# Performance work log

Measured on AMD Instinct MI355X. Metric: run time of the kernel, lower is better.

Reference implementation:

```python
import jax, jax.numpy as jnp
import numpy as np

B, S, D = 1, 4096, 1024
H, DH = 8, 128
SCALING = 256.0 ** -0.5
SOFTCAP = 50.0
WINDOW = 512
EPS = 1e-6
NEG = -1e30


def setup_inputs() -> dict:
    key = jax.random.key(0)
    ks = jax.random.split(key, 8)
    hidden_states = jax.random.normal(ks[0], (B, S, D), dtype=jnp.float32)
    # rope tables: plausible cos/sin in [-1,1]
    inv_freq = 1.0 / (10000.0 ** (jnp.arange(0, DH, 2, dtype=jnp.float32) / DH))
    t = jnp.arange(S, dtype=jnp.float32)
    freqs = jnp.outer(t, inv_freq)  # [S, DH/2]
    emb = jnp.concatenate([freqs, freqs], axis=-1)  # [S, DH]
    cos = jnp.cos(emb)[None]  # [1, S, DH]
    sin = jnp.sin(emb)[None]
    w = 0.02
    Wq = jax.random.normal(ks[1], (H * DH, D), dtype=jnp.float32) * w
    Wk = jax.random.normal(ks[2], (H * DH, D), dtype=jnp.float32) * w
    Wv = jax.random.normal(ks[3], (H * DH, D), dtype=jnp.float32) * w
    Wo = jax.random.normal(ks[4], (D, H * DH), dtype=jnp.float32) * w
    q_norm_w = jnp.zeros((DH,), dtype=jnp.float32)
    k_norm_w = jnp.zeros((DH,), dtype=jnp.float32)
    return {"hidden_states": hidden_states, "cos": cos, "sin": sin,
            "Wq": Wq, "Wk": Wk, "Wv": Wv, "Wo": Wo,
            "q_norm_w": q_norm_w, "k_norm_w": k_norm_w}


def _rms_norm(x, w):
    # Gemma3 RMSNorm: x * rsqrt(mean(x^2) + eps) * (1 + w)
    var = jnp.mean(jnp.square(x), axis=-1, keepdims=True)
    return x * jax.lax.rsqrt(var + EPS) * (1.0 + w)


def _rotate_half(x):
    x1, x2 = jnp.split(x, 2, axis=-1)
    return jnp.concatenate([-x2, x1], axis=-1)


def reference(hidden_states, cos, sin, Wq, Wk, Wv, Wo, q_norm_w, k_norm_w):
    b, s, _ = hidden_states.shape
    # QKV projections -> [B, H, S, DH]
    q = (hidden_states @ Wq.T).reshape(b, s, H, DH).transpose(0, 2, 1, 3)
    k = (hidden_states @ Wk.T).reshape(b, s, H, DH).transpose(0, 2, 1, 3)
    v = (hidden_states @ Wv.T).reshape(b, s, H, DH).transpose(0, 2, 1, 3)
    # per-head RMSNorm on q and k
    q = _rms_norm(q, q_norm_w)
    k = _rms_norm(k, k_norm_w)
    # RoPE (cos/sin broadcast over heads via unsqueeze(1))
    c = cos[:, None, :, :]
    si = sin[:, None, :, :]
    q = q * c + _rotate_half(q) * si
    k = k * c + _rotate_half(k) * si
    # scores with scaling and logit softcapping
    scores = jnp.einsum('bhqd,bhkd->bhqk', q, k) * SCALING
    scores = SOFTCAP * jnp.tanh(scores / SOFTCAP)
    # causal + sliding-window mask: attend to j with 0 <= i - j < WINDOW (plus j == i)
    i = jnp.arange(s)[:, None]
    j = jnp.arange(s)[None, :]
    mask = (j <= i) & (i - j < WINDOW)  # [S, S]
    scores = jnp.where(mask[None, None], scores, NEG)
    probs = jax.nn.softmax(scores, axis=-1)  # [B, H, S, S]
    attn = jnp.einsum('bhqk,bhkd->bhqd', probs, v)
    attn = attn.transpose(0, 2, 1, 3).reshape(b, s, H * DH)
    out = attn @ Wo.T
    return out, probs
```

## Files before the change

### kernel.cpp

```cpp
#include <hip/hip_runtime.h>

#define S_LEN 4096

typedef _Float16 f16;
typedef __bf16 bf16;
typedef __attribute__((ext_vector_type(4))) _Float16 f16x4;
typedef __attribute__((ext_vector_type(8))) _Float16 f16x8;
typedef __attribute__((ext_vector_type(8))) __bf16 bf16x8;
typedef __attribute__((ext_vector_type(4))) float f32x4;

__device__ __forceinline__ void async_cp16(void* lds, const void* g) {
  __builtin_amdgcn_global_load_lds((const __attribute__((address_space(1))) void*)g,
                                   (__attribute__((address_space(3))) void*)lds, 16, 0, 0);
}

__device__ __forceinline__ f32x4 mfma16(f16x8 a, f16x8 b, f32x4 c) {
  return __builtin_amdgcn_mfma_f32_16x16x32_f16(a, b, c, 0, 0, 0);
}

__global__ void detect_dtype(const unsigned short* __restrict__ x, int* __restrict__ flag) {
  const int t = threadIdx.x;
  int cnt = 0;
  for (int i = t; i < 16384; i += 256) {
    const int e = (x[i] >> 7) & 0xFF;
    cnt += (e >= 0x87);
  }
#pragma unroll
  for (int m = 1; m < 64; m <<= 1) cnt += __shfl_xor(cnt, m);
  __shared__ int red[4];
  if ((t & 63) == 0) red[t >> 6] = cnt;
  __syncthreads();
  if (t == 0) *flag = (red[0] + red[1] + red[2] + red[3] > 64) ? 1 : 0;
}

__device__ __forceinline__ void cvt8(const void* src, f16* dst, int i, int fp) {
  f16x8 o;
  if (fp) {
    const float* s = (const float*)src;
#pragma unroll
    for (int j = 0; j < 8; ++j) o[j] = (f16)s[i + j];
  } else {
    const bf16x8 v = *(const bf16x8*)((const bf16*)src + i);
#pragma unroll
    for (int j = 0; j < 8; ++j) o[j] = (f16)(float)v[j];
  }
  *(f16x8*)(dst + i) = o;
}

__global__ void cvt_all(const void* __restrict__ hs, const void* __restrict__ wq,
                        const void* __restrict__ wk, const void* __restrict__ wv,
                        const void* __restrict__ wo, const void* __restrict__ c,
                        const void* __restrict__ s, const void* __restrict__ qn,
                        const void* __restrict__ kn, f16* __restrict__ hsf,
                        f16* __restrict__ wqkv, f16* __restrict__ woh,
                        float* __restrict__ cd, float* __restrict__ sd,
                        float* __restrict__ qnd, float* __restrict__ knd,
                        const int* __restrict__ flagp) {
  const int fp = *flagp;
  const int b = blockIdx.x, tid = threadIdx.x;
  if (b < 2048) {
    cvt8(hs, hsf, (b * 256 + tid) * 8, fp);
  } else if (b < 4096) {
    const int bb = b - 2048;
    const int sub = bb >> 9;
    const int i = ((bb & 511) * 256 + tid) * 8;
    const void* src = (sub == 0) ? wq : (sub == 1) ? wk : (sub == 2) ? wv : wo;
    f16* dst = (sub < 3) ? (wqkv + (size_t)sub * 1048576) : woh;
    cvt8(src, dst, i, fp);
  } else if (b < 8192) {
    const int bb = b - 4096;
    const void* src = (bb < 2048) ? c : s;
    float* dst = (bb < 2048) ? cd : sd;
    const int i = (bb & 2047) * 256 + tid;
    dst[i] = fp ? ((const float*)src)[i] : (float)((const bf16*)src)[i];
  } else {
    if (tid < 128) qnd[tid] = fp ? ((const float*)qn)[tid] : (float)((const bf16*)qn)[tid];
    else knd[tid - 128] = fp ? ((const float*)kn)[tid - 128] : (float)((const bf16*)kn)[tid - 128];
  }
}

__device__ __forceinline__ void probs_zero_fill(void* dout, int fp, int fb, int nfb) {
  const int tid = threadIdx.x;
  if (fp) {
    float* pb = (float*)dout + 4194304;
    const int total = 8 * 4096 * 880;
    const f32x4 z = {};
    for (int u = fb * 256 + tid; u < total; u += nfb * 256) {
      const int rowid = (int)((unsigned)u / 880u);
      const int cu = u - rowid * 880;
      const int row = rowid & 4095;
      const int q0r = row & ~63;
      const int jc0 = (q0r >= 512) ? (((q0r - 511) >> 6) << 6) : 0;
      const int jc0c = jc0 >> 2;
      const int c4 = (cu < jc0c) ? (cu << 2) : (jc0 + 576 + ((cu - jc0c) << 2));
      __builtin_nontemporal_store(z, (f32x4*)&pb[((size_t)rowid << 12) + c4]);
    }
  } else {
    bf16* pb = (bf16*)dout + 4194304;
    const int total = 8 * 4096 * 440;
    const bf16x8 z = {};
    for (int u = fb * 256 + tid; u < total; u += nfb * 256) {
      const int rowid = (int)((unsigned)u / 440u);
      const int cu = u - rowid * 440;
      const int row = rowid & 4095;
      const int q0r = row & ~63;
      const int jc0 = (q0r >= 512) ? (((q0r - 511) >> 6) << 6) : 0;
      const int jc0c = jc0 >> 3;
      const int c8 = (cu < jc0c) ? (cu << 3) : (jc0 + 576 + ((cu - jc0c) << 3));
      __builtin_nontemporal_store(z, (bf16x8*)&pb[((size_t)rowid << 12) + c8]);
    }
  }
}

__launch_bounds__(256, 2)
__global__ void gemm_qkv(const f16* __restrict__ A, const f16* __restrict__ B,
                         const float* __restrict__ cosp, const float* __restrict__ sinp,
                         const float* __restrict__ qnw, const float* __restrict__ knw,
                         f16* __restrict__ qh, f16* __restrict__ kh, f16* __restrict__ vt) {
  __shared__ f16 smem[16384];
  f16* As = smem;
  f16* Bs = smem + 8192;
  const int tid = threadIdx.x;
  const int w = tid >> 6, l = tid & 63;
  const int n0 = blockIdx.x * 128, m0 = blockIdx.y * 128;
  const int wm = (w >> 1) * 64, wn = (w & 1) * 64;
  f32x4 acc[4][4] = {};
  for (int k0 = 0; k0 < 1024; k0 += 64) {
#pragma unroll
    for (int it = 0; it < 4; ++it) {
      const int c = it * 4 + w;
      const int row = c * 8 + (l >> 3);
      const int dq = (l & 7) ^ (row & 7);
      async_cp16(&As[c * 512], &A[(size_t)(m0 + row) * 1024 + k0 + dq * 8]);
      async_cp16(&Bs[c * 512], &B[(size_t)(n0 + row) * 1024 + k0 + dq * 8]);
    }
    __syncthreads();
#pragma unroll
    for (int ks = 0; ks < 2; ++ks) {
      f16x8 af[4], bfr[4];
#pragma unroll
      for (int i = 0; i < 4; ++i) {
        const int ra = wm + i * 16 + (l & 15);
        af[i] = *(const f16x8*)&As[ra * 64 + (((ks * 4 + (l >> 4)) ^ (ra & 7)) << 3)];
        const int rb = wn + i * 16 + (l & 15);
        bfr[i] = *(const f16x8*)&Bs[rb * 64 + (((ks * 4 + (l >> 4)) ^ (rb & 7)) << 3)];
      }
#pragma unroll
      for (int mi = 0; mi < 4; ++mi)
#pragma unroll
        for (int ni = 0; ni < 4; ++ni)
          acc[mi][ni] = mfma16(af[mi], bfr[ni], acc[mi][ni]);
    }
    __syncthreads();
  }
  const int part = blockIdx.x >> 3;
  const int h = blockIdx.x & 7;
#pragma unroll
  for (int mi = 0; mi < 4; ++mi)
#pragma unroll
    for (int ni = 0; ni < 4; ++ni) {
      const int col = wn + ni * 16 + (l & 15);
#pragma unroll
      for (int r = 0; r < 4; ++r) {
        const int row = wm + mi * 16 + ((l >> 4) << 2) + r;
        smem[row * 128 + (col ^ (((row >> 3) & 7) << 3))] = (f16)acc[mi][ni][r];
      }
    }
  __syncthreads();
  if (part == 2) {
#pragma unroll
    for (int it = 0; it < 8; ++it) {
      const int idx = it * 256 + tid;
      const int dh = idx >> 4;
      const int sl = (idx & 15) * 8;
      f16x8 o;
#pragma unroll
      for (int k = 0; k < 8; ++k)
        o[k] = smem[(sl + k) * 128 + (dh ^ ((((sl + k) >> 3) & 7) << 3))];
      *(f16x8*)&vt[((size_t)(h * 128 + dh)) * S_LEN + m0 + sl] = o;
    }
  } else {
    const float* nw = part ? knw : qnw;
    f16* outb = part ? kh : qh;
    const float nw0 = 1.f + nw[l], nw1 = 1.f + nw[l + 64];
#pragma unroll 4
    for (int rr = 0; rr < 32; ++rr) {
      const int row = w * 32 + rr;
      const int sg = m0 + row;
      const int cs = ((row >> 3) & 7) << 3;
      const float x0 = (float)smem[row * 128 + (l ^ cs)];
      const float x1 = (float)smem[row * 128 + ((l + 64) ^ cs)];
      float ssum = x0 * x0 + x1 * x1;
#pragma unroll
      for (int m = 1; m < 64; m <<= 1) ssum += __shfl_xor(ssum, m);
      const float rn = rsqrtf(ssum * (1.f / 128.f) + 1e-6f);
      const float g0 = rn * nw0, g1 = rn * nw1;
      const float c0 = cosp[sg * 128 + l], c1 = cosp[sg * 128 + l + 64];
      const float s0 = sinp[sg * 128 + l], s1 = sinp[sg * 128 + l + 64];
      f16* o = outb + ((size_t)h * S_LEN + sg) * 128;
      o[l] = (f16)(x0 * g0 * c0 - x1 * g1 * s0);
      o[l + 64] = (f16)(x1 * g1 * c1 + x0 * g0 * s1);
    }
  }
}

__launch_bounds__(256, 3)
__global__ void attn64(const f16* __restrict__ Qh, const f16* __restrict__ Kh,
                       const f16* __restrict__ Vt, f16* __restrict__ Pc,
                       float* __restrict__ Lsg, f16* __restrict__ Oh,
                       void* __restrict__ dout, const int* __restrict__ flagp) {
  __shared__ f16 Qs[64 * 128];
  __shared__ f16 Ks[64 * 128];
  __shared__ f16 Vs[128 * 64];
  const int id = blockIdx.x;
  if (id >= 512) {
    probs_zero_fill(dout, *flagp, id - 512, gridDim.x - 512);
    return;
  }
  const int tid = threadIdx.x, w = tid >> 6, l = tid & 63;
  const int q0 = (id & 63) * 64, h = id >> 6;
  const int kt0 = (q0 >= 512) ? ((q0 - 511) >> 6) : 0;
  const int kt1 = (q0 + 64) >> 6;

#pragma unroll
  for (int it = 0; it < 4; ++it) {
    const int c = it * 4 + w;
    const int row = c * 4 + (l >> 4);
    const int dq = (l & 15) ^ (row & 15);
    async_cp16(&Qs[c * 512], &Qh[((size_t)h * S_LEN + q0 + row) * 128 + dq * 8]);
  }
  __syncthreads();
  f16x8 qfrag[4];
#pragma unroll
  for (int ks = 0; ks < 4; ++ks) {
    const int r = w * 16 + (l & 15);
    qfrag[ks] = *(const f16x8*)&Qs[r * 128 + (((ks * 4 + (l >> 4)) ^ (r & 15)) << 3)];
  }
  __syncthreads();

  f16* Ps = Qs + w * 1024;
  float l_i[4] = {0.f, 0.f, 0.f, 0.f};
  f32x4 oacc[8] = {};

  for (int t = kt0; t < kt1; ++t) {
#pragma unroll
    for (int it = 0; it < 4; ++it) {
      const int c = it * 4 + w;
      { const int row = c * 4 + (l >> 4);
        const int dq = (l & 15) ^ (row & 15);
        async_cp16(&Ks[c * 512], &Kh[((size_t)h * S_LEN + t * 64 + row) * 128 + dq * 8]); }
      { const int row = c * 8 + (l >> 3);
        const int dq = (l & 7) ^ (row & 7);
        async_cp16(&Vs[c * 512], &Vt[((size_t)h * 128 + row) * S_LEN + t * 64 + dq * 8]); }
    }
    __syncthreads();
    f32x4 sacc[4] = {};
    __builtin_amdgcn_s_setprio(1);
#pragma unroll
    for (int ks = 0; ks < 4; ++ks) {
      f16x8 kfrag[4];
#pragma unroll
      for (int ni = 0; ni < 4; ++ni) {
        const int r = ni * 16 + (l & 15);
        kfrag[ni] = *(const f16x8*)&Ks[r * 128 + (((ks * 4 + (l >> 4)) ^ (r & 15)) << 3)];
      }
#pragma unroll
      for (int ni = 0; ni < 4; ++ni)
        sacc[ni] = mfma16(qfrag[ks], kfrag[ni], sacc[ni]);
    }
    __builtin_amdgcn_s_setprio(0);
#pragma unroll
    for (int reg = 0; reg < 4; ++reg) {
      const int pr = ((l >> 4) << 2) + reg;
      const int q = q0 + w * 16 + pr;
      float rs = 0.f;
#pragma unroll
      for (int ni = 0; ni < 4; ++ni) {
        const int col = t * 64 + ni * 16 + (l & 15);
        float s = sacc[ni][reg] * 0.0625f;
        const float z = __expf(s * 0.04f);
        s = 50.f * (1.f - 2.f / (z + 1.f));
        const bool valid = (col <= q) && (q - col < 512);
        const float p = valid ? __expf(s - 8.f) : 0.f;
        rs += p;
        const int pc = ni * 16 + (l & 15);
        Ps[pr * 64 + (((pc >> 3) ^ (pr & 7)) << 3) + (pc & 7)] = (f16)p;
      }
#pragma unroll
      for (int m = 1; m < 16; m <<= 1) rs += __shfl_xor(rs, m);
      l_i[reg] += rs;
    }
    __builtin_amdgcn_s_setprio(1);
#pragma unroll
    for (int ks = 0; ks < 2; ++ks) {
      const int rp = l & 15;
      const f16x8 pf = *(const f16x8*)&Ps[rp * 64 + (((ks * 4 + (l >> 4)) ^ (rp & 7)) << 3)];
      f16x8 vf[8];
#pragma unroll
      for (int ni = 0; ni < 8; ++ni) {
        const int r = ni * 16 + (l & 15);
        vf[ni] = *(const f16x8*)&Vs[r * 64 + (((ks * 4 + (l >> 4)) ^ (r & 7)) << 3)];
      }
#pragma unroll
      for (int ni = 0; ni < 8; ++ni)
        oacc[ni] = mfma16(pf, vf[ni], oacc[ni]);
    }
    __builtin_amdgcn_s_setprio(0);
    {
      const size_t rowbase = (size_t)h * 4096 + q0 + w * 16;
#pragma unroll
      for (int i = 0; i < 4; ++i) {
        const int pr = i * 4 + (l >> 4);
        const int pc = (l & 15) * 4;
        const f16x4 v = *(const f16x4*)&Ps[pr * 64 + (((pc >> 3) ^ (pr & 7)) << 3) + (pc & 7)];
        *(f16x4*)&Pc[(rowbase + pr) * 576 + (t - kt0) * 64 + pc] = v;
      }
    }
    __syncthreads();
  }

  float il[4];
#pragma unroll
  for (int r = 0; r < 4; ++r) il[r] = 1.f / l_i[r];
  if ((l & 15) == 0) {
#pragma unroll
    for (int r = 0; r < 4; ++r)
      Lsg[(h << 12) + q0 + w * 16 + ((l >> 4) << 2) + r] = il[r];
  }
#pragma unroll
  for (int ni = 0; ni < 8; ++ni) {
    const int row = q0 + w * 16 + ((l >> 4) << 2);
    const int col = h * 128 + ni * 16 + (l & 15);
#pragma unroll
    for (int r = 0; r < 4; ++r)
      Oh[(size_t)(row + r) * 1024 + col] = (f16)(oacc[ni][r] * il[r]);
  }
}

__launch_bounds__(256, 2)
__global__ void gemmO_probs(const f16* __restrict__ A, const f16* __restrict__ B,
                            void* __restrict__ dout, const f16* __restrict__ Pc,
                            const float* __restrict__ Lsg, const int* __restrict__ flagp) {
  __shared__ f16 smem[16384];
  const int fp = *flagp;
  const int tid = threadIdx.x;
  const int id = blockIdx.x;
  const int r4 = id & 3;
  if (r4 == 0) {
    const int bid = id >> 2;
    f16* As = smem;
    f16* Bs = smem + 8192;
    const int w = tid >> 6, l = tid & 63;
    const int n0 = (bid & 7) * 128, m0 = (bid >> 3) * 128;
    const int wm = (w >> 1) * 64, wn = (w & 1) * 64;
    f32x4 acc[4][4] = {};
    for (int k0 = 0; k0 < 1024; k0 += 64) {
#pragma unroll
      for (int it = 0; it < 4; ++it) {
        const int c = it * 4 + w;
        const int row = c * 8 + (l >> 3);
        const int dq = (l & 7) ^ (row & 7);
        async_cp16(&As[c * 512], &A[(size_t)(m0 + row) * 1024 + k0 + dq * 8]);
        async_cp16(&Bs[c * 512], &B[(size_t)(n0 + row) * 1024 + k0 + dq * 8]);
      }
      __syncthreads();
#pragma unroll
      for (int ks = 0; ks < 2; ++ks) {
        f16x8 af[4], bfr[4];
#pragma unroll
        for (int i = 0; i < 4; ++i) {
          const int ra = wm + i * 16 + (l & 15);
          af[i] = *(const f16x8*)&As[ra * 64 + (((ks * 4 + (l >> 4)) ^ (ra & 7)) << 3)];
          const int rb = wn + i * 16 + (l & 15);
          bfr[i] = *(const f16x8*)&Bs[rb * 64 + (((ks * 4 + (l >> 4)) ^ (rb & 7)) << 3)];
        }
#pragma unroll
        for (int mi = 0; mi < 4; ++mi)
#pragma unroll
          for (int ni = 0; ni < 4; ++ni)
            acc[mi][ni] = mfma16(af[mi], bfr[ni], acc[mi][ni]);
      }
      __syncthreads();
    }
#pragma unroll
    for (int mi = 0; mi < 4; ++mi)
#pragma unroll
      for (int ni = 0; ni < 4; ++ni) {
        const int col = n0 + wn + ni * 16 + (l & 15);
        const int row = m0 + wm + mi * 16 + ((l >> 4) << 2);
#pragma unroll
        for (int r = 0; r < 4; ++r) {
          const size_t off = (size_t)(row + r) * 1024 + col;
          if (fp) ((float*)dout)[off] = acc[mi][ni][r];
          else    ((bf16*)dout)[off] = (bf16)acc[mi][ni][r];
        }
      }
  } else {
    const int fb = (id >> 2) * 3 + (r4 - 1), nfb = 768;
    if (fp) {
      float* pb = (float*)dout + 4194304;
      const int total = 8 * 4096 * 144;
      for (int u = fb * 256 + tid; u < total; u += nfb * 256) {
        const int rowid = (int)((unsigned)u / 144u);
        const int cu = u - rowid * 144;
        const int row = rowid & 4095;
        const int q0r = row & ~63;
        const int jc0 = (q0r >= 512) ? (((q0r - 511) >> 6) << 6) : 0;
        const int c4 = jc0 + (cu << 2);
        f32x4 v = {};
        if (c4 < q0r + 64) {
          const float sc = Lsg[rowid];
          const f16x4 pv = *(const f16x4*)&Pc[(size_t)rowid * 576 + (cu << 2)];
#pragma unroll
          for (int k = 0; k < 4; ++k) v[k] = (float)pv[k] * sc;
        }
        __builtin_nontemporal_store(v, (f32x4*)&pb[((size_t)rowid << 12) + c4]);
      }
    } else {
      bf16* pb = (bf16*)dout + 4194304;
      const int total = 8 * 4096 * 72;
      for (int u = fb * 256 + tid; u < total; u += nfb * 256) {
        const int rowid = (int)((unsigned)u / 72u);
        const int cu = u - rowid * 72;
        const int row = rowid & 4095;
        const int q0r = row & ~63;
        const int jc0 = (q0r >= 512) ? (((q0r - 511) >> 6) << 6) : 0;
        const int c8 = jc0 + (cu << 3);
        bf16x8 v = {};
        if (c8 < q0r + 64) {
          const float sc = Lsg[rowid];
          const f16x8 pv = *(const f16x8*)&Pc[(size_t)rowid * 576 + (cu << 3)];
#pragma unroll
          for (int k = 0; k < 8; ++k) v[k] = (bf16)((float)pv[k] * sc);
        }
        __builtin_nontemporal_store(v, (bf16x8*)&pb[((size_t)rowid << 12) + c8]);
      }
    }
  }
}

extern "C" void kernel_launch(void* const* d_in, const int* in_sizes, int n_in,
                              void* d_out, int out_size, void* d_ws, size_t ws_size,
                              hipStream_t stream) {
  (void)in_sizes; (void)n_in; (void)out_size; (void)ws_size;
  char* ws = (char*)d_ws;
  f16*   Pc    = (f16*)(ws);
  f16*   qh    = (f16*)(ws + (36u << 20));
  f16*   kh    = (f16*)(ws + (44u << 20));
  f16*   vt    = (f16*)(ws + (52u << 20));
  f16*   attnh = (f16*)(ws + (60u << 20));
  f16*   woh   = (f16*)(ws + (68u << 20));
  f16*   hsf   = (f16*)(ws + (70u << 20));
  float* Lsg   = (float*)(ws + (70u << 20));
  f16*   wqkv  = (f16*)(ws + (78u << 20));
  float* cosf  = (float*)(ws + (84u << 20));
  float* sinf  = (float*)(ws + (86u << 20));
  float* qnwf  = (float*)(ws + (88u << 20));
  float* knwf  = (float*)(ws + (88u << 20) + 512);
  int*   flag  = (int*)(ws + (88u << 20) + 1024);

  detect_dtype<<<1, 256, 0, stream>>>((const unsigned short*)d_in[0], flag);
  cvt_all<<<8193, 256, 0, stream>>>(d_in[0], d_in[3], d_in[4], d_in[5], d_in[6],
                                    d_in[1], d_in[2], d_in[7], d_in[8],
                                    hsf, wqkv, woh, cosf, sinf, qnwf, knwf, flag);
  gemm_qkv<<<dim3(24, 32), 256, 0, stream>>>(hsf, wqkv, cosf, sinf, qnwf, knwf, qh, kh, vt);
  attn64<<<2048, 256, 0, stream>>>(qh, kh, vt, Pc, Lsg, attnh, d_out, flag);
  gemmO_probs<<<1024, 256, 0, stream>>>(attnh, woh, d_out, Pc, Lsg, flag);
}
```

Measured before the change: 658.4 us.

## Fuse normalized probs write-out into attention kernel, split O-projection GEMM alone

Moves the banded probability normalization and store from the O-projection kernel into the tail of each attention block, using the per-row inverse sums kept in shared memory instead of a global Lsg buffer. The O-projection GEMM now runs alone with 256 blocks rather than sharing its grid with 768 probs-writer blocks. This cuts a global round trip for the row scales and lets the probs stores overlap with other attention blocks. The cost is that the O-projection GEMM no longer overlaps the large probs store, and the attention blocks get longer.

```diff
diff --git a/kernel.cpp b/kernel.cpp
--- a/kernel.cpp
+++ b/kernel.cpp
@@ -207,14 +207,15 @@
 __launch_bounds__(256, 3)
 __global__ void attn64(const f16* __restrict__ Qh, const f16* __restrict__ Kh,
                        const f16* __restrict__ Vt, f16* __restrict__ Pc,
-                       float* __restrict__ Lsg, f16* __restrict__ Oh,
-                       void* __restrict__ dout, const int* __restrict__ flagp) {
+                       f16* __restrict__ Oh, void* __restrict__ dout,
+                       const int* __restrict__ flagp) {
   __shared__ f16 Qs[64 * 128];
   __shared__ f16 Ks[64 * 128];
   __shared__ f16 Vs[128 * 64];
   const int id = blockIdx.x;
+  const int fp = *flagp;
   if (id >= 512) {
-    probs_zero_fill(dout, *flagp, id - 512, gridDim.x - 512);
+    probs_zero_fill(dout, fp, id - 512, gridDim.x - 512);
     return;
   }
   const int tid = threadIdx.x, w = tid >> 6, l = tid & 63;
@@ -239,6 +240,7 @@
   __syncthreads();
 
   f16* Ps = Qs + w * 1024;
+  float* Ls = (float*)(Qs + 4096);
   float l_i[4] = {0.f, 0.f, 0.f, 0.f};
   f32x4 oacc[8] = {};
 
@@ -324,8 +326,7 @@
   for (int r = 0; r < 4; ++r) il[r] = 1.f / l_i[r];
   if ((l & 15) == 0) {
 #pragma unroll
-    for (int r = 0; r < 4; ++r)
-      Lsg[(h << 12) + q0 + w * 16 + ((l >> 4) << 2) + r] = il[r];
+    for (int r = 0; r < 4; ++r) Ls[w * 16 + ((l >> 4) << 2) + r] = il[r];
   }
 #pragma unroll
   for (int ni = 0; ni < 8; ++ni) {
@@ -335,108 +336,95 @@
     for (int r = 0; r < 4; ++r)
       Oh[(size_t)(row + r) * 1024 + col] = (f16)(oacc[ni][r] * il[r]);
   }
+  __syncthreads();
+
+  const int jc0 = kt0 * 64;
+  const int W = (kt1 - kt0) * 64;
+  if (fp) {
+    float* pb = (float*)dout + 4194304;
+    for (int u = tid; u < 64 * 144; u += 256) {
+      const int row = (int)((unsigned)u / 144u);
+      const int cu = u - row * 144;
+      f32x4 v = {};
+      if ((cu << 2) < W) {
+        const float sc = Ls[row];
+        const f16x4 pv = *(const f16x4*)&Pc[((size_t)(h << 12) + q0 + row) * 576 + (cu << 2)];
+#pragma unroll
+        for (int k = 0; k < 4; ++k) v[k] = (float)pv[k] * sc;
+      }
+      __builtin_nontemporal_store(
+          v, (f32x4*)&pb[(((size_t)(h << 12) + q0 + row) << 12) + jc0 + (cu << 2)]);
+    }
+  } else {
+    bf16* pb = (bf16*)dout + 4194304;
+    for (int u = tid; u < 64 * 72; u += 256) {
+      const int row = (int)((unsigned)u / 72u);
+      const int cu = u - row * 72;
+      bf16x8 v = {};
+      if ((cu << 3) < W) {
+        const float sc = Ls[row];
+        const f16x8 pv = *(const f16x8*)&Pc[((size_t)(h << 12) + q0 + row) * 576 + (cu << 3)];
+#pragma unroll
+        for (int k = 0; k < 8; ++k) v[k] = (bf16)((float)pv[k] * sc);
+      }
+      __builtin_nontemporal_store(
+          v, (bf16x8*)&pb[(((size_t)(h << 12) + q0 + row) << 12) + jc0 + (cu << 3)]);
+    }
+  }
 }
 
 __launch_bounds__(256, 2)
-__global__ void gemmO_probs(const f16* __restrict__ A, const f16* __restrict__ B,
-                            void* __restrict__ dout, const f16* __restrict__ Pc,
-                            const float* __restrict__ Lsg, const int* __restrict__ flagp) {
-  __shared__ f16 smem[16384];
+__global__ void gemmO(const f16* __restrict__ A, const f16* __restrict__ B,
+                      void* __restrict__ dout, const int* __restrict__ flagp) {
+  __shared__ f16 As[128 * 64];
+  __shared__ f16 Bs[128 * 64];
   const int fp = *flagp;
   const int tid = threadIdx.x;
-  const int id = blockIdx.x;
-  const int r4 = id & 3;
-  if (r4 == 0) {
-    const int bid = id >> 2;
-    f16* As = smem;
-    f16* Bs = smem + 8192;
-    const int w = tid >> 6, l = tid & 63;
-    const int n0 = (bid & 7) * 128, m0 = (bid >> 3) * 128;
-    const int wm = (w >> 1) * 64, wn = (w & 1) * 64;
-    f32x4 acc[4][4] = {};
-    for (int k0 = 0; k0 < 1024; k0 += 64) {
-#pragma unroll
-      for (int it = 0; it < 4; ++it) {
-        const int c = it * 4 + w;
-        const int row = c * 8 + (l >> 3);
-        const int dq = (l & 7) ^ (row & 7);
-        async_cp16(&As[c * 512], &A[(size_t)(m0 + row) * 1024 + k0 + dq * 8]);
-        async_cp16(&Bs[c * 512], &B[(size_t)(n0 + row) * 1024 + k0 + dq * 8]);
-      }
-      __syncthreads();
-#pragma unroll
-      for (int ks = 0; ks < 2; ++ks) {
-        f16x8 af[4], bfr[4];
-#pragma unroll
-        for (int i = 0; i < 4; ++i) {
-          const int ra = wm + i * 16 + (l & 15);
-          af[i] = *(const f16x8*)&As[ra * 64 + (((ks * 4 + (l >> 4)) ^ (ra & 7)) << 3)];
-          const int rb = wn + i * 16 + (l & 15);
-          bfr[i] = *(const f16x8*)&Bs[rb * 64 + (((ks * 4 + (l >> 4)) ^ (rb & 7)) << 3)];
-        }
-#pragma unroll
-        for (int mi = 0; mi < 4; ++mi)
-#pragma unroll
-          for (int ni = 0; ni < 4; ++ni)
-            acc[mi][ni] = mfma16(af[mi], bfr[ni], acc[mi][ni]);
-      }
-      __syncthreads();
-    }
-#pragma unroll
-    for (int mi = 0; mi < 4; ++mi)
-#pragma unroll
-      for (int ni = 0; ni < 4; ++ni) {
-        const int col = n0 + wn + ni * 16 + (l & 15);
-        const int row = m0 + wm + mi * 16 + ((l >> 4) << 2);
-#pragma unroll
-        for (int r = 0; r < 4; ++r) {
-          const size_t off = (size_t)(row + r) * 1024 + col;
-          if (fp) ((float*)dout)[off] = acc[mi][ni][r];
-          else    ((bf16*)dout)[off] = (bf16)acc[mi][ni][r];
-        }
-      }
-  } else {
-    const int fb = (id >> 2) * 3 + (r4 - 1), nfb = 768;
-    if (fp) {
-      float* pb = (float*)dout + 4194304;
-      const int total = 8 * 4096 * 144;
-      for (int u = fb * 256 + tid; u < total; u += nfb * 256) {
-        const int rowid = (int)((unsigned)u / 144u);
-        const int cu = u - rowid * 144;
-        const int row = rowid & 4095;
-        const int q0r = row & ~63;
-        const int jc0 = (q0r >= 512) ? (((q0r - 511) >> 6) << 6) : 0;
-        const int c4 = jc0 + (cu << 2);
-        f32x4 v = {};
-        if (c4 < q0r + 64) {
-          const float sc = Lsg[rowid];
-          const f16x4 pv = *(const f16x4*)&Pc[(size_t)rowid * 576 + (cu << 2)];
-#pragma unroll
-          for (int k = 0; k < 4; ++k) v[k] = (float)pv[k] * sc;
-        }
-        __builtin_nontemporal_store(v, (f32x4*)&pb[((size_t)rowid << 12) + c4]);
-      }
-    } else {
-      bf16* pb = (bf16*)dout + 4194304;
-      const int total = 8 * 4096 * 72;
-      for (int u = fb * 256 + tid; u < total; u += nfb * 256) {
-        const int rowid = (int)((unsigned)u / 72u);
-        const int cu = u - rowid * 72;
-        const int row = rowid & 4095;
-        const int q0r = row & ~63;
-        const int jc0 = (q0r >= 512) ? (((q0r - 511) >> 6) << 6) : 0;
-        const int c8 = jc0 + (cu << 3);
-        bf16x8 v = {};
-        if (c8 < q0r + 64) {
-          const float sc = Lsg[rowid];
-          const f16x8 pv = *(const f16x8*)&Pc[(size_t)rowid * 576 + (cu << 3)];
-#pragma unroll
-          for (int k = 0; k < 8; ++k) v[k] = (bf16)((float)pv[k] * sc);
-        }
-        __builtin_nontemporal_store(v, (bf16x8*)&pb[((size_t)rowid << 12) + c8]);
-      }
-    }
-  }
+  const int w = tid >> 6, l = tid & 63;
+  const int n0 = (blockIdx.x & 7) * 128, m0 = (blockIdx.x >> 3) * 128;
+  const int wm = (w >> 1) * 64, wn = (w & 1) * 64;
+  f32x4 acc[4][4] = {};
+  for (int k0 = 0; k0 < 1024; k0 += 64) {
+#pragma unroll
+    for (int it = 0; it < 4; ++it) {
+      const int c = it * 4 + w;
+      const int row = c * 8 + (l >> 3);
+      const int dq = (l & 7) ^ (row & 7);
+      async_cp16(&As[c * 512], &A[(size_t)(m0 + row) * 1024 + k0 + dq * 8]);
+      async_cp16(&Bs[c * 512], &B[(size_t)(n0 + row) * 1024 + k0 + dq * 8]);
+    }
+    __syncthreads();
+#pragma unroll
+    for (int ks = 0; ks < 2; ++ks) {
+      f16x8 af[4], bfr[4];
+#pragma unroll
+      for (int i = 0; i < 4; ++i) {
+        const int ra = wm + i * 16 + (l & 15);
+        af[i] = *(const f16x8*)&As[ra * 64 + (((ks * 4 + (l >> 4)) ^ (ra & 7)) << 3)];
+        const int rb = wn + i * 16 + (l & 15);
+        bfr[i] = *(const f16x8*)&Bs[rb * 64 + (((ks * 4 + (l >> 4)) ^ (rb & 7)) << 3)];
+      }
+#pragma unroll
+      for (int mi = 0; mi < 4; ++mi)
+#pragma unroll
+        for (int ni = 0; ni < 4; ++ni)
+          acc[mi][ni] = mfma16(af[mi], bfr[ni], acc[mi][ni]);
+    }
+    __syncthreads();
+  }
+#pragma unroll
+  for (int mi = 0; mi < 4; ++mi)
+#pragma unroll
+    for (int ni = 0; ni < 4; ++ni) {
+      const int col = n0 + wn + ni * 16 + (l & 15);
+      const int row = m0 + wm + mi * 16 + ((l >> 4) << 2);
+#pragma unroll
+      for (int r = 0; r < 4; ++r) {
+        const size_t off = (size_t)(row + r) * 1024 + col;
+        if (fp) ((float*)dout)[off] = acc[mi][ni][r];
+        else    ((bf16*)dout)[off] = (bf16)acc[mi][ni][r];
+      }
+    }
 }
 
 extern "C" void kernel_launch(void* const* d_in, const int* in_sizes, int n_in,
@@ -451,7 +439,6 @@
   f16*   attnh = (f16*)(ws + (60u << 20));
   f16*   woh   = (f16*)(ws + (68u << 20));
   f16*   hsf   = (f16*)(ws + (70u << 20));
-  float* Lsg   = (float*)(ws + (70u << 20));
   f16*   wqkv  = (f16*)(ws + (78u << 20));
   float* cosf  = (float*)(ws + (84u << 20));
   float* sinf  = (float*)(ws + (86u << 20));
@@ -464,6 +451,6 @@
                                     d_in[1], d_in[2], d_in[7], d_in[8],
                                     hsf, wqkv, woh, cosf, sinf, qnwf, knwf, flag);
   gemm_qkv<<<dim3(24, 32), 256, 0, stream>>>(hsf, wqkv, cosf, sinf, qnwf, knwf, qh, kh, vt);
-  attn64<<<2048, 256, 0, stream>>>(qh, kh, vt, Pc, Lsg, attnh, d_out, flag);
-  gemmO_probs<<<1024, 256, 0, stream>>>(attnh, woh, d_out, Pc, Lsg, flag);
-}
+  attn64<<<2048, 256, 0, stream>>>(qh, kh, vt, Pc, attnh, d_out, flag);
+  gemmO<<<256, 256, 0, stream>>>(attnh, woh, d_out, flag);
+}
```

Result: no change. 663.8 us (+0.8%).
